# Kernel tuning notes

Measured on AMD Instinct MI355X. Metric: run time of the kernel, lower is better.

## Reference

```python
import jax, jax.numpy as jnp
import numpy as np

B, DIM, H = 262144, 8, 100


def setup_inputs() -> dict:
    key = jax.random.key(0)
    ks = jax.random.split(key, 11)
    zt1 = jax.random.normal(ks[0], (B, DIM), dtype=jnp.float32)
    zt2 = zt1 + 0.05 * jax.random.normal(ks[1], (B, DIM), dtype=jnp.float32)
    dt = 0.01 * jnp.ones((B,), dtype=jnp.float32)
    s_in = 1.0 / np.sqrt(DIM)
    s_h = 1.0 / np.sqrt(H)
    # drift MLP: Linear(dim,100) -> Softplus -> Linear(100,dim)
    W1m = jax.random.normal(ks[2], (H, DIM), dtype=jnp.float32) * s_in
    b1m = jax.random.normal(ks[3], (H,), dtype=jnp.float32) * s_in
    W2m = jax.random.normal(ks[4], (DIM, H), dtype=jnp.float32) * s_h
    b2m = jax.random.normal(ks[5], (DIM,), dtype=jnp.float32) * s_h
    # diffusion net: Linear(dim,100) -> Softplus -> Linear(100,dim)  (diag=True -> n_entries=dim)
    W1d = jax.random.normal(ks[6], (H, DIM), dtype=jnp.float32) * s_in
    b1d = jax.random.normal(ks[7], (H,), dtype=jnp.float32) * s_in
    W2d = jax.random.normal(ks[8], (DIM, H), dtype=jnp.float32) * s_h
    b2d = jax.random.normal(ks[9], (DIM,), dtype=jnp.float32) * s_h
    return dict(zt1=zt1, zt2=zt2, dt=dt, W1m=W1m, b1m=b1m, W2m=W2m, b2m=b2m,
                W1d=W1d, b1d=b1d, W2d=W2d, b2d=b2d)


def reference(zt1, zt2, dt, W1m, b1m, W2m, b2m, W1d, b1d, W2d, b2d):
    dt0 = dt[0]
    # drift: mu = MLP(zt1) * dt
    mu = jnp.dot(jax.nn.softplus(jnp.dot(zt1, W1m.T) + b1m), W2m.T) + b2m  # [B, dim]
    mu = mu * dt0
    # diffusion: D = exp(Dnet(zt1)); diag Cholesky L = diag(D)
    D = jnp.exp(jnp.dot(jax.nn.softplus(jnp.dot(zt1, W1d.T) + b1d), W2d.T) + b2d)  # [B, dim]
    dz = zt2 - zt1
    # diag=True: cov = diag(D^2), precision = diag(1/D^2), logdet(cov) = 2*sum(log D)
    inv_var = 1.0 / (D * D)
    t1 = 2.0 * jnp.sum(jnp.log(D), axis=-1)
    t2 = jnp.sum(dz * dz * inv_var, axis=-1)
    t3 = -2.0 * jnp.sum(dz * mu * inv_var, axis=-1)
    t4 = jnp.sum(mu * mu * inv_var, axis=-1)
    const = jnp.asarray(-DIM / 2.0 * np.log(2.0 * np.pi), dtype=zt1.dtype)
    log_pz2 = const - 0.5 * (t1 + t2 + t3 + t4)
    loss = jnp.sum(-log_pz2)
    return loss, mu, D * jnp.sqrt(dt0)
```

## Files before the change

kernel.cpp:

```cpp
#include <hip/hip_runtime.h>

constexpr int BN = 262144;
constexpr int H_ = 100;
constexpr int HHALF = 50;
constexpr int RS = 36;

typedef float v2f __attribute__((ext_vector_type(2)));

__global__ __launch_bounds__(256) void pack_w(
    const float* __restrict__ W1m, const float* __restrict__ b1m,
    const float* __restrict__ W2m, const float* __restrict__ W1d,
    const float* __restrict__ b1d, const float* __restrict__ W2d,
    float* __restrict__ rows)
{
    constexpr float LOG2E = 1.4426950408889634f;
    constexpr float LN2   = 0.6931471805599453f;
    const int gid = blockIdx.x * 256 + threadIdx.x;
    const int NT  = gridDim.x * 256;
    for (int idx = gid; idx < 800; idx += NT) {
        const int j = idx >> 3, k = idx & 7;
        rows[j * RS + 0 + k] = W1m[idx] * LOG2E;
        rows[j * RS + 8 + k] = W1d[idx] * LOG2E;
    }
    for (int idx = gid; idx < 800; idx += NT) {
        const int k = idx / 100, j = idx - k * 100;
        rows[j * RS + 16 + k] = W2m[idx] * LN2;
        rows[j * RS + 24 + k] = W2d[idx] * LN2;
    }
    if (gid < H_) {
        rows[gid * RS + 32] = b1m[gid] * LOG2E;
        rows[gid * RS + 33] = b1d[gid] * LOG2E;
    }
}

__global__ __launch_bounds__(256) void sde_fused(
    const float* __restrict__ zt1, const float* __restrict__ zt2,
    const float* __restrict__ dtp, const float* __restrict__ b2m,
    const float* __restrict__ b2d, const float* __restrict__ rows,
    float* __restrict__ out)
{
    __shared__ float xch[256 * 9];
    __shared__ float wsum[4];

    const int tid  = threadIdx.x;
    const int lane = tid & 63;
    const int wv   = tid >> 6;
    const int pair = wv >> 1;
    const int h    = __builtin_amdgcn_readfirstlane(wv & 1);
    const int row  = blockIdx.x * 128 + pair * 64 + lane;

    const float dt0  = dtp[0];
    const float sqdt = sqrtf(dt0);

    v2f xv[4];
    float x[8];
    {
        const float4* p = reinterpret_cast<const float4*>(zt1) + (size_t)row * 2;
        float4 a = p[0], b = p[1];
        x[0]=a.x; x[1]=a.y; x[2]=a.z; x[3]=a.w;
        x[4]=b.x; x[5]=b.y; x[6]=b.z; x[7]=b.w;
        xv[0] = (v2f){a.x, a.y}; xv[1] = (v2f){a.z, a.w};
        xv[2] = (v2f){b.x, b.y}; xv[3] = (v2f){b.z, b.w};
    }
    float4 z2a, z2b;
    {
        const float4* p = reinterpret_cast<const float4*>(zt2) + (size_t)row * 2;
        z2a = p[0]; z2b = p[1];
    }

    v2f amv[4], adv[4];
    if (h == 0) {
        #pragma unroll
        for (int q = 0; q < 4; ++q) {
            amv[q] = (v2f){b2m[2*q], b2m[2*q+1]};
            adv[q] = (v2f){b2d[2*q], b2d[2*q+1]};
        }
    } else {
        #pragma unroll
        for (int q = 0; q < 4; ++q) { amv[q] = (v2f){0.f, 0.f}; adv[q] = (v2f){0.f, 0.f}; }
    }

    const float* __restrict__ rbase = rows + h * (HHALF * RS);
    #pragma unroll 2
    for (int jj = 0; jj < HHALF; ++jj) {
        const float* r = rbase + jj * RS;
        const v2f* rv = reinterpret_cast<const v2f*>(r);
        v2f pmv = (v2f){0.f, 0.f}, pdv = (v2f){0.f, 0.f};
        #pragma unroll
        for (int q = 0; q < 4; ++q) {
            pmv = __builtin_elementwise_fma(xv[q], rv[q],     pmv);
            pdv = __builtin_elementwise_fma(xv[q], rv[4 + q], pdv);
        }
        const float pm = (pmv.x + pmv.y) + r[32];
        const float pd = (pdv.x + pdv.y) + r[33];
        const float hm = log2f(1.0f + exp2f(pm));
        const float hd = log2f(1.0f + exp2f(pd));
        const v2f hm2 = (v2f){hm, hm};
        const v2f hd2 = (v2f){hd, hd};
        #pragma unroll
        for (int q = 0; q < 4; ++q) {
            amv[q] = __builtin_elementwise_fma(hm2, rv[8 + q],  amv[q]);
            adv[q] = __builtin_elementwise_fma(hd2, rv[12 + q], adv[q]);
        }
    }

    float* mine = &xch[tid * 9];
    if (h == 0) {
        mine[0]=amv[2].x; mine[1]=amv[2].y; mine[2]=amv[3].x; mine[3]=amv[3].y;
        mine[4]=adv[2].x; mine[5]=adv[2].y; mine[6]=adv[3].x; mine[7]=adv[3].y;
    } else {
        mine[0]=amv[0].x; mine[1]=amv[0].y; mine[2]=amv[1].x; mine[3]=amv[1].y;
        mine[4]=adv[0].x; mine[5]=adv[0].y; mine[6]=adv[1].x; mine[7]=adv[1].y;
    }
    __syncthreads();
    const float* part = &xch[(tid ^ 64) * 9];

    float* __restrict__ mu_out = out + 1;
    float* __restrict__ sg_out = out + 1 + (size_t)BN * 8;

    float t1 = 0.f, t2 = 0.f, t3 = 0.f, t4 = 0.f;

#define EPI(K0, A0, A1, D0, D1, ZB)                                          \
    {                                                                        \
        const float amk[4] = {A0.x, A0.y, A1.x, A1.y};                       \
        const float adk[4] = {D0.x, D0.y, D1.x, D1.y};                       \
        const float z2v[4] = {ZB.x, ZB.y, ZB.z, ZB.w};                       \
        _Pragma("unroll")                                                    \
        for (int q = 0; q < 4; ++q) {                                        \
            const int k = K0 + q;                                            \
            const float a_m = amk[q] + part[q];                              \
            const float a_d = adk[q] + part[4 + q];                          \
            const float mu = a_m * dt0;                                      \
            const float y  = a_d;                        \
            const float Dk = __expf(y);                                      \
            const float iv = __expf(-2.0f * y);                   \
            const float dz = z2v[q] - x[k];                                  \
            t1 += y;                                                         \
            t2 = fmaf(dz * dz, iv, t2);                                      \
            t3 = fmaf(dz * mu, iv, t3);                                      \
            t4 = fmaf(mu * mu, iv, t4);                                      \
            mu_out[(size_t)row * 8 + k] = mu;                                \
            sg_out[(size_t)row * 8 + k] = Dk * sqdt;                         \
        }                                                                    \
    }

    if (h == 0) { EPI(0, amv[0], amv[1], adv[0], adv[1], z2a) }
    else        { EPI(4, amv[2], amv[3], adv[2], adv[3], z2b) }
#undef EPI

    float nll = fmaf(0.5f, (2.0f * t1 + t2 - 2.0f * t3 + t4),
                     3.67575413281869039f);

    #pragma unroll
    for (int off = 32; off > 0; off >>= 1) nll += __shfl_down(nll, off);

    if (lane == 0) wsum[wv] = nll;
    __syncthreads();
    if (tid == 0) atomicAdd(out, wsum[0] + wsum[1] + wsum[2] + wsum[3]);
}

extern "C" void kernel_launch(void* const* d_in, const int* in_sizes, int n_in,
                              void* d_out, int out_size, void* d_ws, size_t ws_size,
                              hipStream_t stream) {
    float* rows = (float*)d_ws;
    hipMemsetAsync(d_out, 0, sizeof(float), stream);
    pack_w<<<4, 256, 0, stream>>>(
        (const float*)d_in[3], (const float*)d_in[4],
        (const float*)d_in[5],
        (const float*)d_in[7], (const float*)d_in[8],
        (const float*)d_in[9],
        rows);
    sde_fused<<<BN / 128, 256, 0, stream>>>(
        (const float*)d_in[0], (const float*)d_in[1], (const float*)d_in[2],
        (const float*)d_in[6], (const float*)d_in[10],
        rows, (float*)d_out);
}
```

Baseline: 135.3 us.

## Process two rows per thread to reuse weight loads across rows

Each thread now computes the MLP for two batch rows at once, so every weight row fetched from global/scalar memory is used for twice as much FMA and transcendental work. The grid is halved, and the zt2 load moves after the hidden-layer loop, fetching only the half each thread needs. The LDS exchange buffer grows to hold both rows' partial sums, and the per-thread constant term is doubled to cover two rows. This trades more registers and less occupancy for fewer weight loads per row and more independent instructions to hide latency.

```diff
diff --git a/kernel.cpp b/kernel.cpp
--- a/kernel.cpp
+++ b/kernel.cpp
@@ -39,7 +39,7 @@
     const float* __restrict__ b2d, const float* __restrict__ rows,
     float* __restrict__ out)
 {
-    __shared__ float xch[256 * 9];
+    __shared__ float xch[256 * 17];
     __shared__ float wsum[4];
 
     const int tid  = threadIdx.x;
@@ -47,37 +47,37 @@
     const int wv   = tid >> 6;
     const int pair = wv >> 1;
     const int h    = __builtin_amdgcn_readfirstlane(wv & 1);
-    const int row  = blockIdx.x * 128 + pair * 64 + lane;
+    const int rowA = blockIdx.x * 256 + pair * 128 + lane;
+    const int rowB = rowA + 64;
 
     const float dt0  = dtp[0];
     const float sqdt = sqrtf(dt0);
 
-    v2f xv[4];
-    float x[8];
+    v2f xA[4], xB[4];
     {
-        const float4* p = reinterpret_cast<const float4*>(zt1) + (size_t)row * 2;
-        float4 a = p[0], b = p[1];
-        x[0]=a.x; x[1]=a.y; x[2]=a.z; x[3]=a.w;
-        x[4]=b.x; x[5]=b.y; x[6]=b.z; x[7]=b.w;
-        xv[0] = (v2f){a.x, a.y}; xv[1] = (v2f){a.z, a.w};
-        xv[2] = (v2f){b.x, b.y}; xv[3] = (v2f){b.z, b.w};
-    }
-    float4 z2a, z2b;
-    {
-        const float4* p = reinterpret_cast<const float4*>(zt2) + (size_t)row * 2;
-        z2a = p[0]; z2b = p[1];
-    }
-
-    v2f amv[4], adv[4];
+        const float4* p = reinterpret_cast<const float4*>(zt1);
+        float4 a0 = p[(size_t)rowA * 2], a1 = p[(size_t)rowA * 2 + 1];
+        float4 b0 = p[(size_t)rowB * 2], b1 = p[(size_t)rowB * 2 + 1];
+        xA[0]=(v2f){a0.x,a0.y}; xA[1]=(v2f){a0.z,a0.w};
+        xA[2]=(v2f){a1.x,a1.y}; xA[3]=(v2f){a1.z,a1.w};
+        xB[0]=(v2f){b0.x,b0.y}; xB[1]=(v2f){b0.z,b0.w};
+        xB[2]=(v2f){b1.x,b1.y}; xB[3]=(v2f){b1.z,b1.w};
+    }
+
+    v2f amA[4], adA[4], amB[4], adB[4];
     if (h == 0) {
         #pragma unroll
         for (int q = 0; q < 4; ++q) {
-            amv[q] = (v2f){b2m[2*q], b2m[2*q+1]};
-            adv[q] = (v2f){b2d[2*q], b2d[2*q+1]};
+            const v2f bm = (v2f){b2m[2*q], b2m[2*q+1]};
+            const v2f bd = (v2f){b2d[2*q], b2d[2*q+1]};
+            amA[q] = bm; adA[q] = bd; amB[q] = bm; adB[q] = bd;
         }
     } else {
         #pragma unroll
-        for (int q = 0; q < 4; ++q) { amv[q] = (v2f){0.f, 0.f}; adv[q] = (v2f){0.f, 0.f}; }
+        for (int q = 0; q < 4; ++q) {
+            amA[q] = (v2f){0.f,0.f}; adA[q] = (v2f){0.f,0.f};
+            amB[q] = (v2f){0.f,0.f}; adB[q] = (v2f){0.f,0.f};
+        }
     }
 
     const float* __restrict__ rbase = rows + h * (HHALF * RS);
@@ -85,71 +85,94 @@
     for (int jj = 0; jj < HHALF; ++jj) {
         const float* r = rbase + jj * RS;
         const v2f* rv = reinterpret_cast<const v2f*>(r);
-        v2f pmv = (v2f){0.f, 0.f}, pdv = (v2f){0.f, 0.f};
-        #pragma unroll
-        for (int q = 0; q < 4; ++q) {
-            pmv = __builtin_elementwise_fma(xv[q], rv[q],     pmv);
-            pdv = __builtin_elementwise_fma(xv[q], rv[4 + q], pdv);
-        }
-        const float pm = (pmv.x + pmv.y) + r[32];
-        const float pd = (pdv.x + pdv.y) + r[33];
-        const float hm = log2f(1.0f + exp2f(pm));
-        const float hd = log2f(1.0f + exp2f(pd));
-        const v2f hm2 = (v2f){hm, hm};
-        const v2f hd2 = (v2f){hd, hd};
-        #pragma unroll
-        for (int q = 0; q < 4; ++q) {
-            amv[q] = __builtin_elementwise_fma(hm2, rv[8 + q],  amv[q]);
-            adv[q] = __builtin_elementwise_fma(hd2, rv[12 + q], adv[q]);
-        }
-    }
-
-    float* mine = &xch[tid * 9];
+        v2f pmA=(v2f){0.f,0.f}, pdA=(v2f){0.f,0.f};
+        v2f pmB=(v2f){0.f,0.f}, pdB=(v2f){0.f,0.f};
+        #pragma unroll
+        for (int q = 0; q < 4; ++q) {
+            pmA = __builtin_elementwise_fma(xA[q], rv[q],     pmA);
+            pmB = __builtin_elementwise_fma(xB[q], rv[q],     pmB);
+            pdA = __builtin_elementwise_fma(xA[q], rv[4 + q], pdA);
+            pdB = __builtin_elementwise_fma(xB[q], rv[4 + q], pdB);
+        }
+        const float pA = (pmA.x + pmA.y) + r[32];
+        const float qA = (pdA.x + pdA.y) + r[33];
+        const float pB = (pmB.x + pmB.y) + r[32];
+        const float qB = (pdB.x + pdB.y) + r[33];
+        const float hmA = log2f(1.0f + exp2f(pA));
+        const float hdA = log2f(1.0f + exp2f(qA));
+        const float hmB = log2f(1.0f + exp2f(pB));
+        const float hdB = log2f(1.0f + exp2f(qB));
+        const v2f hmA2=(v2f){hmA,hmA}, hdA2=(v2f){hdA,hdA};
+        const v2f hmB2=(v2f){hmB,hmB}, hdB2=(v2f){hdB,hdB};
+        #pragma unroll
+        for (int q = 0; q < 4; ++q) {
+            amA[q] = __builtin_elementwise_fma(hmA2, rv[8 + q],  amA[q]);
+            amB[q] = __builtin_elementwise_fma(hmB2, rv[8 + q],  amB[q]);
+            adA[q] = __builtin_elementwise_fma(hdA2, rv[12 + q], adA[q]);
+            adB[q] = __builtin_elementwise_fma(hdB2, rv[12 + q], adB[q]);
+        }
+    }
+
+    const float4* z2p = reinterpret_cast<const float4*>(zt2);
+    const float4 zA = z2p[(size_t)rowA * 2 + h];
+    const float4 zB = z2p[(size_t)rowB * 2 + h];
+
+    float* mine = &xch[tid * 17];
     if (h == 0) {
-        mine[0]=amv[2].x; mine[1]=amv[2].y; mine[2]=amv[3].x; mine[3]=amv[3].y;
-        mine[4]=adv[2].x; mine[5]=adv[2].y; mine[6]=adv[3].x; mine[7]=adv[3].y;
+        mine[0]=amA[2].x; mine[1]=amA[2].y; mine[2]=amA[3].x; mine[3]=amA[3].y;
+        mine[4]=adA[2].x; mine[5]=adA[2].y; mine[6]=adA[3].x; mine[7]=adA[3].y;
+        mine[8]=amB[2].x; mine[9]=amB[2].y; mine[10]=amB[3].x; mine[11]=amB[3].y;
+        mine[12]=adB[2].x; mine[13]=adB[2].y; mine[14]=adB[3].x; mine[15]=adB[3].y;
     } else {
-        mine[0]=amv[0].x; mine[1]=amv[0].y; mine[2]=amv[1].x; mine[3]=amv[1].y;
-        mine[4]=adv[0].x; mine[5]=adv[0].y; mine[6]=adv[1].x; mine[7]=adv[1].y;
+        mine[0]=amA[0].x; mine[1]=amA[0].y; mine[2]=amA[1].x; mine[3]=amA[1].y;
+        mine[4]=adA[0].x; mine[5]=adA[0].y; mine[6]=adA[1].x; mine[7]=adA[1].y;
+        mine[8]=amB[0].x; mine[9]=amB[0].y; mine[10]=amB[1].x; mine[11]=amB[1].y;
+        mine[12]=adB[0].x; mine[13]=adB[0].y; mine[14]=adB[1].x; mine[15]=adB[1].y;
     }
     __syncthreads();
-    const float* part = &xch[(tid ^ 64) * 9];
+    const float* part = &xch[(tid ^ 64) * 17];
 
     float* __restrict__ mu_out = out + 1;
     float* __restrict__ sg_out = out + 1 + (size_t)BN * 8;
 
     float t1 = 0.f, t2 = 0.f, t3 = 0.f, t4 = 0.f;
 
-#define EPI(K0, A0, A1, D0, D1, ZB)                                          \
+#define EPI(K0, A0, A1, D0, D1, X0, X1, Z, PB, ROW)                          \
     {                                                                        \
         const float amk[4] = {A0.x, A0.y, A1.x, A1.y};                       \
         const float adk[4] = {D0.x, D0.y, D1.x, D1.y};                       \
-        const float z2v[4] = {ZB.x, ZB.y, ZB.z, ZB.w};                       \
+        const float xk[4]  = {X0.x, X0.y, X1.x, X1.y};                       \
+        const float z2v[4] = {Z.x, Z.y, Z.z, Z.w};                           \
         _Pragma("unroll")                                                    \
         for (int q = 0; q < 4; ++q) {                                        \
             const int k = K0 + q;                                            \
-            const float a_m = amk[q] + part[q];                              \
-            const float a_d = adk[q] + part[4 + q];                          \
+            const float a_m = amk[q] + part[PB + q];                         \
+            const float a_d = adk[q] + part[PB + 4 + q];                     \
             const float mu = a_m * dt0;                                      \
             const float y  = a_d;                        \
             const float Dk = __expf(y);                                      \
             const float iv = __expf(-2.0f * y);                   \
-            const float dz = z2v[q] - x[k];                                  \
+            const float dz = z2v[q] - xk[q];                                 \
             t1 += y;                                                         \
             t2 = fmaf(dz * dz, iv, t2);                                      \
             t3 = fmaf(dz * mu, iv, t3);                                      \
             t4 = fmaf(mu * mu, iv, t4);                                      \
-            mu_out[(size_t)row * 8 + k] = mu;                                \
-            sg_out[(size_t)row * 8 + k] = Dk * sqdt;                         \
+            mu_out[(size_t)(ROW) * 8 + k] = mu;                              \
+            sg_out[(size_t)(ROW) * 8 + k] = Dk * sqdt;                       \
         }                                                                    \
     }
 
-    if (h == 0) { EPI(0, amv[0], amv[1], adv[0], adv[1], z2a) }
-    else        { EPI(4, amv[2], amv[3], adv[2], adv[3], z2b) }
+    if (h == 0) {
+        EPI(0, amA[0], amA[1], adA[0], adA[1], xA[0], xA[1], zA, 0, rowA)
+        EPI(0, amB[0], amB[1], adB[0], adB[1], xB[0], xB[1], zB, 8, rowB)
+    } else {
+        EPI(4, amA[2], amA[3], adA[2], adA[3], xA[2], xA[3], zA, 0, rowA)
+        EPI(4, amB[2], amB[3], adB[2], adB[3], xB[2], xB[3], zB, 8, rowB)
+    }
 #undef EPI
 
     float nll = fmaf(0.5f, (2.0f * t1 + t2 - 2.0f * t3 + t4),
-                     3.67575413281869039f);
+                     7.3515082656373808f);
 
     #pragma unroll
     for (int off = 32; off > 0; off >>= 1) nll += __shfl_down(nll, off);
@@ -170,7 +193,7 @@
         (const float*)d_in[7], (const float*)d_in[8],
         (const float*)d_in[9],
         rows);
-    sde_fused<<<BN / 128, 256, 0, stream>>>(
+    sde_fused<<<BN / 256, 256, 0, stream>>>(
         (const float*)d_in[0], (const float*)d_in[1], (const float*)d_in[2],
         (const float*)d_in[6], (const float*)d_in[10],
         rows, (float*)d_out);
```

New measurement: 129.6 us. 1.04x faster.
